# Kernel optimization log

Measured on AMD Instinct MI355X. Metric: run time of the kernel, lower is better.

Reference implementation:

```python
import jax, jax.numpy as jnp
from jax import lax
import numpy as np
import math

B, T, D_IN, H, L, NDIR = 32, 512, 1024, 512, 2, 2


def setup_inputs() -> dict:
    key = jax.random.key(0)
    ks = jax.random.split(key, 5)
    std = 1.0 / math.sqrt(H)  # torch init: uniform(-std, std)
    u = lambda k, shape: jax.random.uniform(k, shape, jnp.float32, -std, std)
    return {
        "x": jax.random.normal(ks[0], (B, T, D_IN), jnp.float32),
        "Wx": u(ks[1], (L, NDIR, D_IN, 4 * H)),   # x2h weight (in, 4H)
        "bx": u(ks[2], (L, NDIR, 4 * H)),
        "Wh": u(ks[3], (L, NDIR, H, 4 * H)),      # h2h weight (H, 4H)
        "bh": u(ks[4], (L, NDIR, 4 * H)),
    }


def _lstm_dir(xs, Wx, bx, Wh, bh):
    """xs: [T,B,Din]; returns hs [T,B,H], (hT, cT)."""
    # precompute input projection for all timesteps (one big GEMM)
    gx = jnp.einsum('tbd,dg->tbg', xs, Wx) + bx + bh  # [T,B,4H]
    h0 = jnp.zeros((xs.shape[1], Wh.shape[0]), xs.dtype)

    def step(carry, gx_t):
        h, c = carry
        gates = gx_t + h @ Wh  # [B,4H]
        i, f, g, o = jnp.split(gates, 4, axis=-1)  # torch chunk order: i,f,g,o
        i = jax.nn.sigmoid(i)
        f = jax.nn.sigmoid(f)
        g = jnp.tanh(g)
        o = jax.nn.sigmoid(o)
        c = c * f + i * g
        h = o * jnp.tanh(c)
        return (h, c), h

    (hT, cT), hs = lax.scan(step, (h0, h0), gx)
    return hs, hT, cT


def reference(x, Wx, bx, Wh, bh):
    # x: [B,T,D_IN] (batch_first) -> time-major
    inputs = jnp.swapaxes(x, 0, 1)  # [T,B,D]
    h_list, c_list = [], []
    for layer in range(L):
        outs_dirs = []
        for d in range(NDIR):
            xs = inputs if d == 0 else inputs[::-1]
            hs, hT, cT = _lstm_dir(xs, Wx[layer, d], bx[layer, d], Wh[layer, d], bh[layer, d])
            outs_dirs.append(hs if d == 0 else hs[::-1])
            h_list.append(hT)
            c_list.append(cT)
        inputs = jnp.concatenate(outs_dirs, axis=-1)  # [T,B,2H] (dropout=0 / eval)
    output = jnp.swapaxes(inputs, 0, 1)  # [B,T,2H]
    h_n = jnp.stack(h_list)  # [L*NDIR, B, H]
    c_n = jnp.stack(c_list)
    return output, h_n, c_n
```

## Files before the change

### kernel.cpp

```cpp
#include <hip/hip_runtime.h>
#include <hip/hip_bf16.h>

#define DEV __device__ __forceinline__

typedef __bf16 bf16;
typedef __bf16 bf16x8 __attribute__((ext_vector_type(8)));
typedef float f32x4 __attribute__((ext_vector_type(4)));
typedef int i32x4 __attribute__((ext_vector_type(4)));
typedef unsigned int u32;
typedef unsigned long long u64;

#define BB 32
#define TT 512
#define DIN 1024
#define HH 512
#define G4 2048
#define MM (TT*BB)
#define TAGMAGIC 0x5A000000u

DEV float sigmf(float x){ return 1.0f/(1.0f + __expf(-x)); }
DEV float tanhfast(float x){ return 1.0f - 2.0f/(__expf(2.0f*x)+1.0f); }

DEV void gload16(const void* g, void* l){
  __builtin_amdgcn_global_load_lds((const __attribute__((address_space(1))) void*)g,
                                   (__attribute__((address_space(3))) void*)l, 16, 0, 0);
}

DEV i32x4 cload16(const void* p){
  i32x4 v;
  asm volatile("global_load_dwordx4 %0, %1, off sc0 sc1"
               : "=&v"(v) : "v"(p) : "memory");
  return v;
}
DEV void cstore16(void* p, i32x4 v){
  asm volatile("global_store_dwordx4 %0, %1, off sc0 sc1"
               :: "v"(p), "v"(v) : "memory");
}
DEV void waitvm0(){ asm volatile("s_waitcnt vmcnt(0)" ::: "memory"); }

__global__ void k_dbg(float* out, float v){ out[0] = v; }

__global__ void k_prep_bias(const float* __restrict__ bx, const float* __restrict__ bh,
                            float* __restrict__ bsum){
  int gid = blockIdx.x*256 + threadIdx.x;
  if (gid < 4*G4) bsum[gid] = bx[gid] + bh[gid];
}

__global__ void k_xswz(const float* __restrict__ x, bf16* __restrict__ xs){
  int gid = blockIdx.x*256 + threadIdx.x;
  int r = gid >> 7, kc = gid & 127;
  int b = r & 31, t = r >> 5;
  const float* px = x + ((size_t)b*TT + t)*DIN + kc*8;
  float4 v0 = *(const float4*)px;
  float4 v1 = *(const float4*)(px+4);
  bf16x8 o;
  o[0]=(bf16)v0.x; o[1]=(bf16)v0.y; o[2]=(bf16)v0.z; o[3]=(bf16)v0.w;
  o[4]=(bf16)v1.x; o[5]=(bf16)v1.y; o[6]=(bf16)v1.z; o[7]=(bf16)v1.w;
  *(bf16x8*)(xs + (size_t)r*DIN + ((kc ^ (r&7))<<3)) = o;
}

__global__ void k_twx(const float* __restrict__ Wx, bf16* __restrict__ Wxt){
  int ld = blockIdx.z;
  int k0 = blockIdx.x*64, n0 = blockIdx.y*64;
  const float* in = Wx + (size_t)ld*DIN*G4;
  bf16* outp = Wxt + (size_t)ld*G4*DIN;
  __shared__ float tile[64][68];
  int tid = threadIdx.x;
  #pragma unroll
  for (int rr=0; rr<4; rr++){
    int row = rr*16 + (tid>>4); int c4 = (tid&15)*4;
    float4 v = *(const float4*)(in + (size_t)(k0+row)*G4 + n0 + c4);
    *(float4*)&tile[row][c4] = v;
  }
  __syncthreads();
  #pragma unroll
  for (int uu=0; uu<2; uu++){
    int u = uu*256 + tid;
    int nn = u>>3, ck = u&7;
    bf16x8 o;
    #pragma unroll
    for (int j=0;j<8;j++) o[j] = (bf16)tile[ck*8+j][nn];
    int ncol = n0 + nn;
    int kcg = (k0>>3) + ck;
    *(bf16x8*)(outp + (size_t)ncol*DIN + ((size_t)(kcg ^ (ncol&7))<<3)) = o;
  }
}

__global__ void k_twh(const float* __restrict__ Wh, bf16* __restrict__ Whb){
  int ld = blockIdx.z;
  int k0 = blockIdx.x*64, n0 = blockIdx.y*64;
  const float* in = Wh + (size_t)ld*HH*G4;
  bf16* outp = Whb + (size_t)ld*G4*HH;
  __shared__ float tile[64][68];
  int tid = threadIdx.x;
  #pragma unroll
  for (int rr=0; rr<4; rr++){
    int row = rr*16 + (tid>>4); int c4 = (tid&15)*4;
    float4 v = *(const float4*)(in + (size_t)(k0+row)*G4 + n0 + c4);
    *(float4*)&tile[row][c4] = v;
  }
  __syncthreads();
  #pragma unroll
  for (int uu=0; uu<2; uu++){
    int u = uu*256 + tid;
    int nn = u>>3, ck = u&7;
    bf16x8 o;
    #pragma unroll
    for (int j=0;j<8;j++) o[j] = (bf16)tile[ck*8+j][nn];
    int n = n0 + nn;
    int q = n >> 9, rem = n & 511;
    int s = rem >> 4, wq = (rem >> 2) & 3, hcv = rem & 3;
    int cc = s*64 + wq*16 + q*4 + hcv;
    *(bf16x8*)(outp + (size_t)cc*HH + k0 + ck*8) = o;
  }
}

__launch_bounds__(256, 1)
__global__ void k_gemmp(const bf16* __restrict__ A, const bf16* __restrict__ Bw,
                        const float* __restrict__ bias, bf16* __restrict__ out){
  int d = blockIdx.z;
  const bf16* Bp = Bw + (size_t)d*G4*DIN;
  const float* bp = bias + d*G4;
  bf16* op = out + (size_t)d*MM*G4;
  int n0 = blockIdx.x*128, r0 = blockIdx.y*128;
  int tid = threadIdx.x, lane = tid&63, w = tid>>6;
  __shared__ __align__(16) bf16 ldsA[128*64];
  __shared__ __align__(16) bf16 ldsB[128*64];
  f32x4 acc[4][4];
  #pragma unroll
  for (int i=0;i<4;i++)
    #pragma unroll
    for (int j=0;j<4;j++) acc[i][j] = (f32x4){0.f,0.f,0.f,0.f};
  int wm = w>>1, wn = w&1;
  for (int kt=0; kt<16; kt++){
    __syncthreads();
    #pragma unroll
    for (int p=0;p<4;p++){
      int seg = p*4 + w;
      int row = seg*8 + (lane>>3);
      int cch = lane&7;
      gload16(A  + (size_t)(r0+row)*DIN + kt*64 + cch*8, ldsA + seg*512);
      gload16(Bp + (size_t)(n0+row)*DIN + kt*64 + cch*8, ldsB + seg*512);
    }
    __syncthreads();
    #pragma unroll
    for (int ks=0; ks<2; ks++){
      bf16x8 af[4], bf_[4];
      #pragma unroll
      for (int at=0; at<4; at++){
        int row = wm*64 + at*16 + (lane&15);
        int ch = (ks*4 + (lane>>4)) ^ (row&7);
        af[at] = *(const bf16x8*)(ldsA + row*64 + ch*8);
      }
      #pragma unroll
      for (int bt=0; bt<4; bt++){
        int col = wn*64 + bt*16 + (lane&15);
        int ch = (ks*4 + (lane>>4)) ^ (col&7);
        bf_[bt] = *(const bf16x8*)(ldsB + col*64 + ch*8);
      }
      #pragma unroll
      for (int at=0; at<4; at++)
        #pragma unroll
        for (int bt=0; bt<4; bt++)
          acc[at][bt] = __builtin_amdgcn_mfma_f32_16x16x32_bf16(af[at], bf_[bt], acc[at][bt], 0,0,0);
    }
  }
  float bv[4];
  #pragma unroll
  for (int bt=0;bt<4;bt++) bv[bt] = bp[n0 + wn*64 + bt*16 + (lane&15)];
  int l4 = lane>>4;
  #pragma unroll
  for (int a=0; a<2; a++){
    int tt = (r0 + wm*64 + a*32) >> 5;
    #pragma unroll
    for (int bt=0; bt<4; bt++){
      int col = n0 + wn*64 + bt*16 + (lane&15);
      int q = col >> 9, rem = col & 511;
      int sD = rem >> 4, wR = (rem >> 2) & 3, hcD = rem & 3;
      int tIdx = wR*64 + l4*16 + q*4 + hcD;
      bf16x8 u8;
      #pragma unroll
      for (int j=0;j<4;j++) u8[j]   = (bf16)(acc[a*2][bt][j]   + bv[bt]);
      #pragma unroll
      for (int j=0;j<4;j++) u8[4+j] = (bf16)(acc[a*2+1][bt][j] + bv[bt]);
      *(bf16x8*)(op + (((size_t)tt*32 + sD)*256 + tIdx)*8) = u8;
    }
  }
}

__launch_bounds__(256, 1)
__global__ void k_rec(const bf16* __restrict__ Whb, const bf16* __restrict__ gx,
                      char* __restrict__ hbT,
                      bf16* __restrict__ out0, float* __restrict__ dout,
                      float* __restrict__ hn, float* __restrict__ cn, int layer){
  int tid = threadIdx.x, lane = tid&63, w = tid>>6;
  int d = blockIdx.x >> 5, s = blockIdx.x & 31;
  __shared__ __align__(16) bf16 hA[32*512];
  __shared__ __align__(8) unsigned short hP[4*128];
  const bf16* Wp = Whb + ((size_t)d*G4 + s*64 + w*16 + (lane&15))*HH;
  bf16x8 bfr[16];
  #pragma unroll
  for (int kk=0; kk<16; kk++) bfr[kk] = *(const bf16x8*)(Wp + kk*32 + (lane>>4)*8);
  float cst[2][4] = {{0,0,0,0},{0,0,0,0}};
  const bf16* gxD = gx + (size_t)d*MM*G4;
  const u32 tagbase = TAGMAGIC + (u32)((layer*2 + d)*TT);
  int q = (lane>>2)&3, hc = lane&3;
  int m0 = lane&15;
  bool hi = (q >= 2), odd = (q & 1);

  for (int t=0; t<TT; t++){
    int tt = d ? (TT-1-t) : t;
    bf16x8 gv = *(const bf16x8*)(gxD + (((size_t)tt*32 + s)*256 + tid)*8);
    f32x4 acc0 = {0.f,0.f,0.f,0.f}, acc1 = {0.f,0.f,0.f,0.f};
    if (t > 0){
      const char* sT = hbT + ((size_t)(d*2 + ((t-1)&1)) << 16);
      u32 want = tagbase + (u32)t;
      i32x4 u[16];
      #pragma unroll
      for (int i=0;i<16;i++){ int g = i*256 + tid; u[i] = cload16(sT + ((size_t)g<<4)); }
      waitvm0();
      __builtin_amdgcn_sched_barrier(0);
      while (true){
        bool bad = false;
        #pragma unroll
        for (int i=0;i<16;i++) bad |= ((u32)u[i].z != want);
        if (!__any(bad)) break;
        __builtin_amdgcn_s_sleep(1);
        #pragma unroll
        for (int i=0;i<16;i++) if ((u32)u[i].z != want){ int g = i*256 + tid; u[i] = cload16(sT + ((size_t)g<<4)); }
        waitvm0();
        __builtin_amdgcn_sched_barrier(0);
      }
      __syncthreads();
      #pragma unroll
      for (int i=0;i<16;i++){
        int g = i*256 + tid; int b = g>>7, cu = g&127;
        u64 dat = ((u64)(u32)u[i].y << 32) | (u32)u[i].x;
        *(u64*)((char*)hA + b*1024 + ((((cu>>1) ^ (b&7)))<<4) + (cu&1)*8) = dat;
      }
      __syncthreads();
      #pragma unroll
      for (int kk=0; kk<16; kk++){
        int ch = (kk*4 + (lane>>4)) ^ (m0&7);
        bf16x8 a0 = *(const bf16x8*)(hA + m0*HH + ch*8);
        bf16x8 a1 = *(const bf16x8*)(hA + (m0+16)*HH + ch*8);
        acc0 = __builtin_amdgcn_mfma_f32_16x16x32_bf16(a0, bfr[kk], acc0, 0,0,0);
        acc1 = __builtin_amdgcn_mfma_f32_16x16x32_bf16(a1, bfr[kk], acc1, 0,0,0);
      }
    }
    #pragma unroll
    for (int mt=0; mt<2; mt++){
      #pragma unroll
      for (int rg=0; rg<4; rg++){
        float gpre = (mt ? acc1[rg] : acc0[rg]) + (float)gv[mt*4+rg];
        float x4  = __shfl_xor(gpre, 4);
        float x8  = __shfl_xor(gpre, 8);
        float x12 = __shfl_xor(gpre, 12);
        float a04 = odd ? x4 : gpre,  b04 = odd ? gpre : x4;
        float a812 = odd ? x12 : x8,  b812 = odd ? x8 : x12;
        float ig = hi ? a812 : a04;
        float fg = hi ? b812 : b04;
        float gg = hi ? a04 : a812;
        float og = hi ? b04 : b812;
        float iv = sigmf(ig), fv = sigmf(fg), gv_ = tanhfast(gg), ov = sigmf(og);
        float c = cst[mt][rg]*fv + iv*gv_;
        cst[mt][rg] = c;
        float hvv = ov * tanhfast(c);
        if (q == 0){
          int b = mt*16 + (lane>>4)*4 + rg;
          hP[w*128 + b*4 + hc] = __builtin_bit_cast(unsigned short, (bf16)hvv);
          if (layer == 1)
            __builtin_nontemporal_store(hvv,
              dout + ((size_t)(b*TT + tt))*(2*HH) + d*HH + s*16 + w*4 + hc);
          if (t == TT-1)
            hn[((size_t)((layer*2+d)*BB + b))*HH + s*16 + w*4 + hc] = hvv;
        }
      }
    }
    if (t == TT-1 && q == 0){
      #pragma unroll
      for (int mt=0; mt<2; mt++)
        #pragma unroll
        for (int rg=0; rg<4; rg++){
          int b = mt*16 + (lane>>4)*4 + rg;
          cn[((size_t)((layer*2+d)*BB + b))*HH + s*16 + w*4 + hc] = cst[mt][rg];
        }
    }
    if (lane < 32){
      u64 d8 = *(const u64*)(hP + w*128 + lane*4);
      if (t < TT-1){
        char* dT = hbT + ((size_t)(d*2 + (t&1)) << 16);
        i32x4 unit;
        unit.x = (int)(u32)(d8 & 0xffffffffu);
        unit.y = (int)(u32)(d8 >> 32);
        unit.z = (int)(tagbase + (u32)t + 1u);
        unit.w = 0;
        cstore16(dT + ((size_t)(lane*128 + s*4 + w) << 4), unit);
      }
      if (layer == 0){
        int r = tt*BB + lane;
        int c = d*64 + s*2 + (w>>1);
        *(u64*)(out0 + (size_t)r*DIN + (size_t)(c ^ (r&7))*8 + (w&1)*4) = d8;
      }
    }
  }
}

extern "C" void kernel_launch(void* const* d_in, const int* in_sizes, int n_in,
                              void* d_out, int out_size, void* d_ws, size_t ws_size,
                              hipStream_t stream){
  const float* x  = (const float*)d_in[0];
  const float* Wx = (const float*)d_in[1];
  const float* bx = (const float*)d_in[2];
  const float* Wh = (const float*)d_in[3];
  const float* bh = (const float*)d_in[4];
  float* outp = (float*)d_out;
  char* ws = (char*)d_ws;

  const size_t szWxt  = (size_t)4*G4*DIN*2;
  const size_t szWhb  = (size_t)4*G4*HH*2;
  const size_t szBsum = (size_t)4*G4*4;
  const size_t szXO   = (size_t)MM*DIN*2;
  const size_t szHbT  = (size_t)2*2*4096*16;
  const size_t szGx   = (size_t)2*MM*G4*2;

  size_t off = 0;
  auto take = [&](size_t b)->size_t{ size_t r = off; off = (off + b + 255) & ~(size_t)255; return r; };
  size_t oWxt = take(szWxt), oWhb = take(szWhb), oBsum = take(szBsum);
  size_t oXO  = take(szXO), oHbT = take(szHbT), oGx = take(szGx);
  if (off > ws_size){
    k_dbg<<<1, 1, 0, stream>>>(outp, (float)((double)ws_size / 1048576.0));
    return;
  }

  bf16* Wxt  = (bf16*)(ws + oWxt);
  bf16* Whb  = (bf16*)(ws + oWhb);
  float* bsum= (float*)(ws + oBsum);
  bf16* xo   = (bf16*)(ws + oXO);
  bf16* out0 = xo;
  char* hbT  = ws + oHbT;
  bf16* gx   = (bf16*)(ws + oGx);

  float* hn = outp + (size_t)BB*TT*2*HH;
  float* cn = hn + (size_t)4*BB*HH;

  hipMemsetAsync(hbT, 0, szHbT, stream);
  k_prep_bias<<<32, 256, 0, stream>>>(bx, bh, bsum);
  k_xswz<<<(MM*128)/256, 256, 0, stream>>>(x, xo);
  k_twx<<<dim3(16,32,4), 256, 0, stream>>>(Wx, Wxt);
  k_twh<<<dim3(8,32,4), 256, 0, stream>>>(Wh, Whb);

  for (int layer=0; layer<2; layer++){
    k_gemmp<<<dim3(16,128,2), 256, 0, stream>>>(xo, Wxt + (size_t)layer*2*G4*DIN,
                                                bsum + layer*2*G4, gx);
    k_rec<<<64, 256, 0, stream>>>(Whb + (size_t)layer*2*G4*HH, gx, hbT,
                                  out0, outp, hn, cn, layer);
  }
}
```

Baseline: 5.766 ms.

## Replace tagged double-buffer handoff with per-timestep sentinel-filled h slots

The recurrent kernel previously exchanged h between blocks through a double-buffered area where each 16-byte unit carried 8 bytes of data plus a tag word, and readers polled the tags. Now every timestep gets its own slot, pre-filled with 0xFF by a memset before each layer. Writers store only 8-byte data, and readers treat any all-ones word as not yet written. This halves the bytes each block polls and removes the tag packing. In exchange, a 32 MB buffer is memset before each layer, and correctness depends on real bf16 data never forming an all-ones dword pattern (NaN bits).

```diff
diff --git a/kernel.cpp b/kernel.cpp
--- a/kernel.cpp
+++ b/kernel.cpp
@@ -16,7 +16,6 @@
 #define HH 512
 #define G4 2048
 #define MM (TT*BB)
-#define TAGMAGIC 0x5A000000u
 
 DEV float sigmf(float x){ return 1.0f/(1.0f + __expf(-x)); }
 DEV float tanhfast(float x){ return 1.0f - 2.0f/(__expf(2.0f*x)+1.0f); }
@@ -32,8 +31,8 @@
                : "=&v"(v) : "v"(p) : "memory");
   return v;
 }
-DEV void cstore16(void* p, i32x4 v){
-  asm volatile("global_store_dwordx4 %0, %1, off sc0 sc1"
+DEV void cstore8(void* p, u64 v){
+  asm volatile("global_store_dwordx2 %0, %1, off sc0 sc1"
                :: "v"(p), "v"(v) : "memory");
 }
 DEV void waitvm0(){ asm volatile("s_waitcnt vmcnt(0)" ::: "memory"); }
@@ -190,8 +189,8 @@
 
 __launch_bounds__(256, 1)
 __global__ void k_rec(const bf16* __restrict__ Whb, const bf16* __restrict__ gx,
-                      char* __restrict__ hbT,
-                      bf16* __restrict__ out0, float* __restrict__ dout,
+                      char* __restrict__ hbS, bf16* __restrict__ out0,
+                      float* __restrict__ dout,
                       float* __restrict__ hn, float* __restrict__ cn, int layer){
   int tid = threadIdx.x, lane = tid&63, w = tid>>6;
   int d = blockIdx.x >> 5, s = blockIdx.x & 31;
@@ -203,7 +202,6 @@
   for (int kk=0; kk<16; kk++) bfr[kk] = *(const bf16x8*)(Wp + kk*32 + (lane>>4)*8);
   float cst[2][4] = {{0,0,0,0},{0,0,0,0}};
   const bf16* gxD = gx + (size_t)d*MM*G4;
-  const u32 tagbase = TAGMAGIC + (u32)((layer*2 + d)*TT);
   int q = (lane>>2)&3, hc = lane&3;
   int m0 = lane&15;
   bool hi = (q >= 2), odd = (q & 1);
@@ -213,30 +211,37 @@
     bf16x8 gv = *(const bf16x8*)(gxD + (((size_t)tt*32 + s)*256 + tid)*8);
     f32x4 acc0 = {0.f,0.f,0.f,0.f}, acc1 = {0.f,0.f,0.f,0.f};
     if (t > 0){
-      const char* sT = hbT + ((size_t)(d*2 + ((t-1)&1)) << 16);
-      u32 want = tagbase + (u32)t;
-      i32x4 u[16];
-      #pragma unroll
-      for (int i=0;i<16;i++){ int g = i*256 + tid; u[i] = cload16(sT + ((size_t)g<<4)); }
+      const char* sS = hbS + ((size_t)(d*TT + (t-1)) << 15);
+      i32x4 u[8];
+      #pragma unroll
+      for (int i=0;i<8;i++) u[i] = cload16(sS + ((size_t)(i*256 + tid) << 4));
       waitvm0();
       __builtin_amdgcn_sched_barrier(0);
-      while (true){
-        bool bad = false;
-        #pragma unroll
-        for (int i=0;i<16;i++) bad |= ((u32)u[i].z != want);
-        if (!__any(bad)) break;
+      u32 valid = 0;
+      #pragma unroll
+      for (int i=0;i<8;i++){
+        bool ok = (u[i].x != -1) && (u[i].y != -1) && (u[i].z != -1) && (u[i].w != -1);
+        valid |= (ok ? 1u : 0u) << i;
+      }
+      while (__any(valid != 0xFFu)){
         __builtin_amdgcn_s_sleep(1);
         #pragma unroll
-        for (int i=0;i<16;i++) if ((u32)u[i].z != want){ int g = i*256 + tid; u[i] = cload16(sT + ((size_t)g<<4)); }
+        for (int i=0;i<8;i++)
+          if (!((valid>>i)&1)) u[i] = cload16(sS + ((size_t)(i*256 + tid) << 4));
         waitvm0();
         __builtin_amdgcn_sched_barrier(0);
+        valid = 0;
+        #pragma unroll
+        for (int i=0;i<8;i++){
+          bool ok = (u[i].x != -1) && (u[i].y != -1) && (u[i].z != -1) && (u[i].w != -1);
+          valid |= (ok ? 1u : 0u) << i;
+        }
       }
       __syncthreads();
       #pragma unroll
-      for (int i=0;i<16;i++){
-        int g = i*256 + tid; int b = g>>7, cu = g&127;
-        u64 dat = ((u64)(u32)u[i].y << 32) | (u32)u[i].x;
-        *(u64*)((char*)hA + b*1024 + ((((cu>>1) ^ (b&7)))<<4) + (cu&1)*8) = dat;
+      for (int i=0;i<8;i++){
+        int g = i*256 + tid; int row = g>>6, uc = g&63;
+        *(i32x4*)((char*)hA + row*1024 + ((uc ^ (row&7))<<4)) = u[i];
       }
       __syncthreads();
       #pragma unroll
@@ -288,15 +293,8 @@
     }
     if (lane < 32){
       u64 d8 = *(const u64*)(hP + w*128 + lane*4);
-      if (t < TT-1){
-        char* dT = hbT + ((size_t)(d*2 + (t&1)) << 16);
-        i32x4 unit;
-        unit.x = (int)(u32)(d8 & 0xffffffffu);
-        unit.y = (int)(u32)(d8 >> 32);
-        unit.z = (int)(tagbase + (u32)t + 1u);
-        unit.w = 0;
-        cstore16(dT + ((size_t)(lane*128 + s*4 + w) << 4), unit);
-      }
+      if (t < TT-1)
+        cstore8(hbS + ((size_t)(d*TT + t) << 15) + (((size_t)lane*128 + s*4 + w) << 3), d8);
       if (layer == 0){
         int r = tt*BB + lane;
         int c = d*64 + s*2 + (w>>1);
@@ -321,13 +319,13 @@
   const size_t szWhb  = (size_t)4*G4*HH*2;
   const size_t szBsum = (size_t)4*G4*4;
   const size_t szXO   = (size_t)MM*DIN*2;
-  const size_t szHbT  = (size_t)2*2*4096*16;
+  const size_t szHbS  = (size_t)2*TT*32768;
   const size_t szGx   = (size_t)2*MM*G4*2;
 
   size_t off = 0;
   auto take = [&](size_t b)->size_t{ size_t r = off; off = (off + b + 255) & ~(size_t)255; return r; };
   size_t oWxt = take(szWxt), oWhb = take(szWhb), oBsum = take(szBsum);
-  size_t oXO  = take(szXO), oHbT = take(szHbT), oGx = take(szGx);
+  size_t oXO  = take(szXO), oHbS = take(szHbS), oGx = take(szGx);
   if (off > ws_size){
     k_dbg<<<1, 1, 0, stream>>>(outp, (float)((double)ws_size / 1048576.0));
     return;
@@ -338,22 +336,23 @@
   float* bsum= (float*)(ws + oBsum);
   bf16* xo   = (bf16*)(ws + oXO);
   bf16* out0 = xo;
-  char* hbT  = ws + oHbT;
+  char* hbS  = ws + oHbS;
   bf16* gx   = (bf16*)(ws + oGx);
 
   float* hn = outp + (size_t)BB*TT*2*HH;
   float* cn = hn + (size_t)4*BB*HH;
 
-  hipMemsetAsync(hbT, 0, szHbT, stream);
   k_prep_bias<<<32, 256, 0, stream>>>(bx, bh, bsum);
   k_xswz<<<(MM*128)/256, 256, 0, stream>>>(x, xo);
   k_twx<<<dim3(16,32,4), 256, 0, stream>>>(Wx, Wxt);
   k_twh<<<dim3(8,32,4), 256, 0, stream>>>(Wh, Whb);
 
   for (int layer=0; layer<2; layer++){
-    k_gemmp<<<dim3(16,128,2), 256, 0, stream>>>(xo, Wxt + (size_t)layer*2*G4*DIN,
+    hipMemsetAsync(hbS, 0xFF, szHbS, stream);
+    const bf16* A = layer ? out0 : xo;
+    k_gemmp<<<dim3(16,128,2), 256, 0, stream>>>(A, Wxt + (size_t)layer*2*G4*DIN,
                                                 bsum + layer*2*G4, gx);
-    k_rec<<<64, 256, 0, stream>>>(Whb + (size_t)layer*2*G4*HH, gx, hbT,
-                                  out0, outp, hn, cn, layer);
-  }
-}
+    k_rec<<<64, 256, 0, stream>>>(Whb + (size_t)layer*2*G4*HH, gx, hbS, out0,
+                                  outp, hn, cn, layer);
+  }
+}
```

After: 5.939 ms. 1.03x slower.
